# Optimization experiments

Hardware: AMD Instinct MI355X
Metric: run time of the kernel (lower is better)

## Reference

```python
import jax, jax.numpy as jnp
import numpy as np

H, L, N1, N2, N3 = 256, 141, 9, 34, 98
B, S = 64, 512

def setup_inputs() -> dict:
    key = jax.random.key(0)
    cnt = [0]
    def nrm(shape, s=0.05):
        cnt[0] += 1
        return jax.random.normal(jax.random.fold_in(key, cnt[0]), shape, jnp.float32) * s
    d = {}
    d['inputs'] = jax.random.randint(jax.random.fold_in(key, 1000), (B, S), 0, 30522)
    d['text_hidden'] = nrm((B, S, 768), 1.0)
    d['label_encoding'] = nrm((L, H), 1.0)
    d['w12'] = (jax.random.uniform(jax.random.fold_in(key, 1001), (N1, N2)) < 0.3).astype(jnp.float32)
    d['w23'] = (jax.random.uniform(jax.random.fold_in(key, 1002), (N2, N3)) < 0.3).astype(jnp.float32)
    d['fre12'] = jax.random.uniform(jax.random.fold_in(key, 1003), (N1, N2), jnp.float32)
    d['fre23'] = jax.random.uniform(jax.random.fold_in(key, 1004), (N2, N3), jnp.float32)
    for name in ['wi1', 'wf1', 'wo1', 'wu1', 'wi2', 'wf2', 'wo2', 'wu2']:
        d[name + '_W'] = nrm((H, H)); d[name + '_b'] = nrm((H,))
    for name in ['ui1', 'uf1', 'uo1', 'uu1', 'ui2', 'uf2', 'uo2', 'uu2']:
        d[name + '_W'] = nrm((H, H))
    d['mix_W'] = nrm((3 * H, H)); d['mix_b'] = nrm((H,))
    d['tt_W'] = nrm((768, H)); d['tt_b'] = nrm((H,))
    d['A'] = nrm((L, L)); d['Wp'] = nrm((H, H))
    d['out_W'] = nrm((L * H, L)); d['out_b'] = nrm((L,))
    return d

def reference(inputs, text_hidden, label_encoding, w12, w23, fre12, fre23,
              wi1_W, wi1_b, wf1_W, wf1_b, wo1_W, wo1_b, wu1_W, wu1_b,
              wi2_W, wi2_b, wf2_W, wf2_b, wo2_W, wo2_b, wu2_W, wu2_b,
              ui1_W, uf1_W, uo1_W, uu1_W, ui2_W, uf2_W, uo2_W, uu2_W,
              mix_W, mix_b, tt_W, tt_b, A, Wp, out_W, out_b):
    sig, tanh = jax.nn.sigmoid, jnp.tanh
    v1 = label_encoding[:N1]          # [N1,H]
    v2 = label_encoding[N1:N1 + N2]   # [N2,H]
    v3 = label_encoding[N1 + N2:]     # [N3,H]
    w21, w32 = w12.T, w23.T
    # --- top-down tree-LSTM (suffix 1) ---
    i11 = sig(v1 @ wi1_W + wi1_b); o11 = sig(v1 @ wo1_W + wo1_b); u11 = tanh(v1 @ wu1_W + wu1_b)
    c11 = i11 * u11; h11 = o11 * tanh(c11)
    h21t = w21 @ h11
    i21 = sig(v2 @ wi1_W + wi1_b + h21t @ ui1_W)
    f21 = sig(v2 @ wf1_W + wf1_b + h21t @ uf1_W)
    o21 = sig(v2 @ wo1_W + wo1_b + h21t @ uo1_W)
    u21 = tanh(v2 @ wu1_W + wu1_b + h21t @ uu1_W)
    c21 = i21 * u21 + f21 * (w21 @ c11); h21 = o21 * tanh(c21)
    h31t = w32 @ h21
    i31 = sig(v3 @ wi1_W + wi1_b + h31t @ ui1_W)
    f31 = sig(v3 @ wf1_W + wf1_b + h31t @ uf1_W)
    o31 = sig(v3 @ wo1_W + wo1_b + h31t @ uo1_W)
    u31 = tanh(v3 @ wu1_W + wu1_b + h31t @ uu1_W)
    c31 = i31 * u31 + f31 * (w32 @ c21); h31 = o31 * tanh(c31)
    # --- bottom-up tree-LSTM (suffix 2) ---
    i32 = sig(v3 @ wi2_W + wi2_b); o32 = sig(v3 @ wo2_W + wo2_b); u32 = tanh(v3 @ wu2_W + wu2_b)
    c32 = i32 * u32; h32 = o32 * tanh(c32)
    h22t = fre23 @ h32
    i22 = sig(v2 @ wi2_W + wi2_b + h22t @ ui2_W)
    f22 = sig((w32 @ v2) @ wf2_W + wf2_b + h32 @ uf2_W)   # [N3,H]
    o22 = sig(v2 @ wo2_W + wo2_b + h22t @ uo2_W)
    u22 = tanh(v2 @ wu2_W + wu2_b + h22t @ uu2_W)
    c22 = i22 * u22 + w23 @ (f22 * c32); h22 = o22 * tanh(c22)
    h12t = fre12 @ h22
    i12 = sig(v1 @ wi2_W + wi2_b + h12t @ ui2_W)
    f12 = sig((w21 @ v1) @ wf2_W + wf2_b + h22 @ uf2_W)   # [N2,H]
    o12 = sig(v1 @ wo2_W + wo2_b + h12t @ uo2_W)
    u12 = tanh(v1 @ wu2_W + wu2_b + h12t @ uu2_W)
    c12 = i12 * u12 + w12 @ (f12 * c22); h12 = o12 * tanh(c12)
    h1 = jnp.concatenate([h11, h12], axis=1)
    h2 = jnp.concatenate([h21, h22], axis=1)
    h3 = jnp.concatenate([h31, h32], axis=1)
    le = jnp.concatenate([h1, h2, h3], axis=0)            # [L,2H]
    temp = jax.nn.relu(A @ label_encoding @ Wp)           # [L,H]
    le = jnp.concatenate([le, temp], axis=1) @ mix_W + mix_b  # [L,H]
    # --- masked cross-attention pooling over text ---
    text = tanh(text_hidden @ tt_W + tt_b)                # [B,S,H]
    att = jnp.einsum('lh,bsh->bls', le, text)             # [B,L,S]
    pad = jnp.where((inputs == 0) | (inputs == 101) | (inputs == 102), -jnp.inf, 0.0).astype(text.dtype)
    att = jax.nn.softmax(att + pad[:, None, :], axis=2)
    features = jnp.einsum('bls,bsh->blh', att, text).reshape(inputs.shape[0], -1)  # [B,L*H]
    return sig(features @ out_W + out_b)                  # [B,L]
```

## Files before the change

kernel.cpp:

```cpp
#include <hip/hip_runtime.h>
#include <math.h>

static constexpr int H = 256, L = 141, N1 = 9, N2 = 34, N3 = 98;
static constexpr int B = 64, S = 512;

typedef __attribute__((ext_vector_type(8))) _Float16 f16x8;
typedef __attribute__((ext_vector_type(4))) float f32x4;

__device__ inline unsigned short f2h(float x) {
    _Float16 h = (_Float16)x;
    return __builtin_bit_cast(unsigned short, h);
}
__device__ inline float sigf(float x) { return 1.f / (1.f + __expf(-x)); }

__device__ inline void gload_lds16(const void* g, void* l) {
    __builtin_amdgcn_global_load_lds(
        (const __attribute__((address_space(1))) void*)g,
        (__attribute__((address_space(3))) void*)l, 16, 0, 0);
}

__global__ __launch_bounds__(256) void conv_ttW(
    const float* __restrict__ W, unsigned short* __restrict__ Bt)
{
    __shared__ unsigned short Tl[32][257];
    const int t = blockIdx.x, tid = threadIdx.x;
    #pragma unroll
    for (int p = 0; p < 32; p++) {
        int lin = p * 256 + tid;
        int r = lin >> 8, c = lin & 255;
        Tl[r][c] = f2h(W[(long)(t * 32 + r) * 256 + c]);
    }
    __syncthreads();
    unsigned short v[32];
    #pragma unroll
    for (int kin = 0; kin < 32; kin++) v[kin] = Tl[kin][tid];
    uint4* dst = (uint4*)(Bt + ((long)t * 256 + tid) * 32);
    #pragma unroll
    for (int q = 0; q < 4; q++) dst[q] = ((const uint4*)v)[q];
}

__global__ __launch_bounds__(512, 4) void text_gemm3(
    const float* __restrict__ Af,
    const unsigned short* __restrict__ Bt,
    const float* __restrict__ bias,
    unsigned short* __restrict__ outH,
    unsigned short* __restrict__ outHT)
{
    __shared__ unsigned short smem[28672];
    unsigned short* As = smem;
    unsigned short* Bs = smem + 4096;
    unsigned short* T  = smem;

    const int tid  = threadIdx.x;
    const int wave = tid >> 6, lane = tid & 63;
    const int quad = lane >> 4, l16 = lane & 15;
    const int m0 = blockIdx.x * 64;
    const int wm = (wave >> 2) * 32;
    const int wn = (wave & 3) * 64;

    const int arow = tid >> 3;
    const int ac16 = tid & 7;
    const float* aSrc = Af + (long)(m0 + arow) * 768 + ac16 * 4;
    const int ac8d = ac16 ^ ((arow & 3) << 1);
    const int aWoff = arow * 32 + ac8d * 4;

    const int bsc = (lane & 3) ^ ((lane >> 3) & 3);
    const long bSrcOff0 = (long)(wave * 32 + (lane >> 2)) * 32 + bsc * 8;
    const long bSrcOff1 = bSrcOff0 + 16 * 32;
    const int bDst0 = (wave * 32) * 32, bDst1 = (wave * 32 + 16) * 32;

    int aro[2], bro[4];
    #pragma unroll
    for (int i = 0; i < 2; i++) {
        int r = wm + i * 16 + l16;
        aro[i] = r * 32 + ((quad * 2) ^ ((r & 3) << 1)) * 4;
    }
    #pragma unroll
    for (int j = 0; j < 4; j++) {
        int n = wn + j * 16 + l16;
        bro[j] = n * 32 + ((quad ^ ((n >> 1) & 3)) << 3);
    }

    f32x4 acc[2][4] = {};
    float4 ar0, ar1;

    auto issueB = [&](int kt, int pb) {
        const unsigned short* src = Bt + (long)kt * 8192;
        unsigned short* d = Bs + pb * 8192;
        gload_lds16(src + bSrcOff0, d + bDst0);
        gload_lds16(src + bSrcOff1, d + bDst1);
    };
    auto writeA = [&](const float4& v, int pa) {
        unsigned int p0 = f2h(v.x) | ((unsigned int)f2h(v.y) << 16);
        unsigned int p1 = f2h(v.z) | ((unsigned int)f2h(v.w) << 16);
        *(uint2*)&As[pa * 2048 + aWoff] = make_uint2(p0, p1);
    };

    ar0 = *(const float4*)(aSrc + 0 * 32);
    issueB(0, 0);
    ar1 = *(const float4*)(aSrc + 1 * 32);
    issueB(1, 1);
    asm volatile("s_waitcnt vmcnt(5)" ::: "memory");
    writeA(ar0, 0);
    asm volatile("s_waitcnt vmcnt(3)" ::: "memory");
    asm volatile("s_waitcnt lgkmcnt(0)" ::: "memory");
    asm volatile("s_barrier" ::: "memory");

    auto body = [&](int t, float4& arIn, float4& arOut, int pa, int pr) {
        int kt2 = (t + 2 <= 23) ? t + 2 : 23;
        arOut = *(const float4*)(aSrc + kt2 * 32);
        f16x8 a[2], b[4];
        const unsigned short* ab = As + pa * 2048;
        const unsigned short* bb = Bs + pr * 8192;
        #pragma unroll
        for (int i = 0; i < 2; i++) a[i] = *(const f16x8*)&ab[aro[i]];
        #pragma unroll
        for (int j = 0; j < 4; j++) b[j] = *(const f16x8*)&bb[bro[j]];
        #pragma unroll
        for (int i = 0; i < 2; i++)
            #pragma unroll
            for (int j = 0; j < 4; j++)
                acc[i][j] = __builtin_amdgcn_mfma_f32_16x16x32_f16(
                    a[i], b[j], acc[i][j], 0, 0, 0);
        asm volatile("s_waitcnt vmcnt(3)" ::: "memory");
        writeA(arIn, pa ^ 1);
        int pw = pr + 2; if (pw >= 3) pw -= 3;
        issueB(kt2, pw);
        asm volatile("s_waitcnt vmcnt(3)" ::: "memory");
        asm volatile("s_waitcnt lgkmcnt(0)" ::: "memory");
        asm volatile("s_barrier" ::: "memory");
    };

    int pr = 0;
    #pragma unroll 1
    for (int t = 0; t < 24; t += 2) {
        body(t,     ar1, ar0, t & 1 ? 1 : 0, pr);
        int pr1 = pr + 1; if (pr1 >= 3) pr1 -= 3;
        body(t + 1, ar0, ar1, 1, pr1);
        pr = pr1 + 1; if (pr >= 3) pr -= 3;
    }
    asm volatile("s_waitcnt vmcnt(0)" ::: "memory");
    __syncthreads();

    float bv[4];
    #pragma unroll
    for (int j = 0; j < 4; j++) bv[j] = bias[wn + j * 16 + l16];

    #pragma unroll
    for (int i = 0; i < 2; i++) {
        #pragma unroll
        for (int j = 0; j < 4; j++) {
            const int mlb = wm + i * 16 + quad * 4;
            const int n   = wn + j * 16 + l16;
            unsigned short hv[4];
            #pragma unroll
            for (int r = 0; r < 4; r++) {
                float v = tanhf(acc[i][j][r] + bv[j]);
                hv[r] = f2h(v);
                outH[(long)(m0 + mlb + r) * 256 + n] = hv[r];
            }
            uint2 p;
            p.x = hv[0] | ((unsigned int)hv[1] << 16);
            p.y = hv[2] | ((unsigned int)hv[3] << 16);
            *(uint2*)&T[n * 72 + mlb] = p;
        }
    }
    __syncthreads();
    {
        const int bb2 = m0 >> 9, s0 = m0 & 511;
        const int n = tid >> 1, half = tid & 1;
        const uint4* src = (const uint4*)&T[n * 72 + half * 32];
        uint4* dst = (uint4*)&outHT[((long)bb2 * 256 + n) * 512 + s0 + half * 32];
        dst[0] = src[0]; dst[1] = src[1];
        dst[2] = src[2]; dst[3] = src[3];
    }
}

__global__ __launch_bounds__(512, 4) void att_logits(
    const unsigned short* __restrict__ le_h,
    const unsigned short* __restrict__ text_h,
    const int* __restrict__ tokens,
    float* __restrict__ att)
{
    __shared__ unsigned short A_s[64 * 256];
    __shared__ unsigned short Bs[3][256 * 32];
    const int tid  = threadIdx.x;
    const int wave = tid >> 6, lane = tid & 63;
    const int quad = lane >> 4, l16 = lane & 15;
    const int s0 = blockIdx.x * 256;
    const int m0 = blockIdx.y * 64;
    const int b  = blockIdx.z;
    const int wm = (wave >> 2) * 32;
    const int wn = (wave & 3) * 64;

    const int bsc = (lane & 3) ^ ((lane >> 3) & 3);
    const long bOff0 = (long)(b * 512 + s0 + wave * 32 + (lane >> 2)) * 256 + bsc * 8;
    const long bOff1 = bOff0 + 16 * 256;
    const int bDst0 = (wave * 32) * 32, bDst1 = bDst0 + 16 * 32;
    auto issueB = [&](int kt, int pb) {
        gload_lds16(text_h + bOff0 + kt * 32, &Bs[pb][bDst0]);
        gload_lds16(text_h + bOff1 + kt * 32, &Bs[pb][bDst1]);
    };

    int abase[2], axm[2], bro[4];
    #pragma unroll
    for (int i = 0; i < 2; i++) {
        int r = wm + i * 16 + l16;
        abase[i] = r * 256; axm[i] = r & 7;
    }
    #pragma unroll
    for (int j = 0; j < 4; j++) {
        int n = wn + j * 16 + l16;
        bro[j] = n * 32 + ((quad ^ ((n >> 1) & 3)) << 3);
    }

    #pragma unroll
    for (int p = 0; p < 4; p++) {
        int row = p * 16 + (tid >> 5);
        int c   = tid & 31;
        int grow = m0 + row; if (grow > L - 1) grow = L - 1;
        gload_lds16(le_h + (long)grow * 256 + ((c ^ (row & 7)) << 3),
                    A_s + p * 4096 + wave * 512);
    }
    issueB(0, 0);
    issueB(1, 1);
    asm volatile("s_waitcnt vmcnt(2)" ::: "memory");
    asm volatile("s_barrier" ::: "memory");

    f32x4 acc[2][4] = {};
    #pragma unroll 1
    for (int t = 0; t < 8; t++) {
        const int pr = t % 3;
        f16x8 a[2], b[4];
        #pragma unroll
        for (int i = 0; i < 2; i++)
            a[i] = *(const f16x8*)&A_s[abase[i] + (((t * 4 + quad) ^ axm[i]) << 3)];
        const unsigned short* bb = &Bs[pr][0];
        #pragma unroll
        for (int j = 0; j < 4; j++) b[j] = *(const f16x8*)&bb[bro[j]];
        #pragma unroll
        for (int i = 0; i < 2; i++)
            #pragma unroll
            for (int j = 0; j < 4; j++)
                acc[i][j] = __builtin_amdgcn_mfma_f32_16x16x32_f16(
                    a[i], b[j], acc[i][j], 0, 0, 0);
        if (t < 7) {
            int kt2 = (t + 2 <= 7) ? t + 2 : 7;
            int pw = (t + 2) % 3;
            issueB(kt2, pw);
            asm volatile("s_waitcnt vmcnt(2)" ::: "memory");
            asm volatile("s_barrier" ::: "memory");
        }
    }
    asm volatile("s_waitcnt vmcnt(0)" ::: "memory");

    float mvv[4];
    #pragma unroll
    for (int j = 0; j < 4; j++) {
        int gs = s0 + wn + j * 16 + l16;
        int tok = tokens[(long)b * 512 + gs];
        mvv[j] = (tok == 0 || tok == 101 || tok == 102) ? 1e30f : 0.f;
    }
    #pragma unroll
    for (int i = 0; i < 2; i++)
        #pragma unroll
        for (int j = 0; j < 4; j++)
            #pragma unroll
            for (int r = 0; r < 4; r++) {
                int gm = m0 + wm + i * 16 + quad * 4 + r;
                if (gm < L) {
                    int gs = s0 + wn + j * 16 + l16;
                    att[(long)b * (L * S) + (long)gm * 512 + gs] =
                        acc[i][j][r] - mvv[j];
                }
            }
}

template<int EPI, bool CONVA, int IM>
__global__ __launch_bounds__(256) void gemm_mfma(
    const void* __restrict__ Aptr, int lda, long strA,
    const unsigned short* __restrict__ Bp, int ldb, long strB,
    float* __restrict__ C, int ldc, long strC,
    int M, int N, int K,
    const float* __restrict__ bias,
    const int* __restrict__ tokens,
    unsigned short* __restrict__ outH,
    unsigned short* __restrict__ outHT,
    int kChunk)
{
    __shared__ unsigned short A_s[32 * IM * 32];
    __shared__ unsigned short B_s[128 * 32];
    const int tid  = threadIdx.x;
    const int wave = tid >> 6, lane = tid & 63;
    const int quad = lane >> 4, l16 = lane & 15;
    const int bz = blockIdx.z;
    const int m0 = blockIdx.y * (32 * IM), n0 = blockIdx.x * 128;
    const int wm = (wave & 1) * (16 * IM), wn = (wave >> 1) * 64;

    long aBase, bBase;
    int kBeg, kEnd;
    if (EPI == 4) { aBase = 0; bBase = 0; kBeg = bz * kChunk; kEnd = kBeg + kChunk; }
    else { aBase = (long)bz * strA; bBase = (long)bz * strB; kBeg = 0; kEnd = K; }

    f32x4 acc[IM][4] = {};

    for (int k0 = kBeg; k0 < kEnd; k0 += 32) {
        if (CONVA) {
            const float* Af = (const float*)Aptr + aBase;
            #pragma unroll
            for (int it = 0; it < IM; it++) {
                int idx = it * 256 + tid;
                int row = idx >> 3, col4 = idx & 7;
                int gm = m0 + row; if (gm > M - 1) gm = M - 1;
                float4 v = *(const float4*)(Af + (long)gm * lda + k0 + col4 * 4);
                unsigned int p0 = f2h(v.x) | ((unsigned int)f2h(v.y) << 16);
                unsigned int p1 = f2h(v.z) | ((unsigned int)f2h(v.w) << 16);
                *(uint2*)&A_s[row * 32 + col4 * 4] = make_uint2(p0, p1);
            }
        } else {
            const unsigned short* Ab = (const unsigned short*)Aptr + aBase;
            #pragma unroll
            for (int t = 0; t < IM / 2; t++) {
                int rowb = wave * (8 * IM) + t * 16;
                int gm = m0 + rowb + (lane >> 2); if (gm > M - 1) gm = M - 1;
                gload_lds16(Ab + (long)gm * lda + k0 + (lane & 3) * 8,
                            &A_s[rowb * 32]);
            }
        }
        #pragma unroll
        for (int t = 0; t < 2; t++) {
            int rowb = wave * 32 + t * 16;
            int gn = n0 + rowb + (lane >> 2); if (gn > N - 1) gn = N - 1;
            gload_lds16(Bp + bBase + (long)gn * ldb + k0 + (lane & 3) * 8,
                        &B_s[rowb * 32]);
        }
        __syncthreads();
        f16x8 a[IM], b[4];
        #pragma unroll
        for (int i = 0; i < IM; i++)
            a[i] = *(const f16x8*)&A_s[(wm + i * 16 + l16) * 32 + quad * 8];
        #pragma unroll
        for (int j = 0; j < 4; j++)
            b[j] = *(const f16x8*)&B_s[(wn + j * 16 + l16) * 32 + quad * 8];
        #pragma unroll
        for (int i = 0; i < IM; i++)
            #pragma unroll
            for (int j = 0; j < 4; j++)
                acc[i][j] = __builtin_amdgcn_mfma_f32_16x16x32_f16(
                    a[i], b[j], acc[i][j], 0, 0, 0);
        __syncthreads();
    }

    #pragma unroll
    for (int i = 0; i < IM; i++) {
        #pragma unroll
        for (int j = 0; j < 4; j++) {
            #pragma unroll
            for (int r = 0; r < 4; r++) {
                int ml = wm + i * 16 + quad * 4 + r;
                int nl = wn + j * 16 + l16;
                int gm = m0 + ml, gn = n0 + nl;
                if (gm >= M || gn >= N) continue;
                float v = acc[i][j][r];
                if (EPI == 2) {
                    int tok = tokens[(long)bz * 512 + gn];
                    if (tok == 0 || tok == 101 || tok == 102) v -= 1e30f;
                    C[(long)bz * strC + (long)gm * ldc + gn] = v;
                } else if (EPI == 3) {
                    outH[(long)bz * strC + (long)gm * ldc + gn] = f2h(v);
                } else {
                    C[(long)bz * strC + (long)gm * ldc + gn] = v;
                }
            }
        }
    }
}

__global__ __launch_bounds__(256) void transp_t64(
    const float* __restrict__ src, unsigned short* __restrict__ dst,
    int R, int C)
{
    __shared__ unsigned short T[64 * 65];
    const int tid = threadIdx.x;
    const int r0 = blockIdx.x * 64, c0 = blockIdx.y * 64;
    #pragma unroll
    for (int p = 0; p < 16; p++) {
        int lin = p * 256 + tid;
        int r = lin >> 6, c = lin & 63;
        int gc = c0 + c;
        float v = (gc < C) ? src[(long)(r0 + r) * C + gc] : 0.f;
        T[c * 65 + r] = f2h(v);
    }
    __syncthreads();
    #pragma unroll
    for (int p = 0; p < 16; p++) {
        int lin = p * 256 + tid;
        int c = lin >> 6, r = lin & 63;
        if (c0 + c < C)
            dst[(long)(c0 + c) * R + r0 + r] = T[c * 65 + r];
    }
}

__global__ __launch_bounds__(256) void gate_pre(
    const float* __restrict__ le,
    const float* W0, const float* W1, const float* W2, const float* W3,
    const float* W4, const float* W5, const float* W6,
    const float* b0, const float* b1, const float* b2, const float* b3,
    const float* b4, const float* b5, const float* b6,
    float* __restrict__ G)
{
    __shared__ float ls[256];
    __shared__ float red[256];
    const int j = blockIdx.x >> 2, x = blockIdx.x & 3, m = blockIdx.y;
    const int tid = threadIdx.x, nl = tid & 63, ks = tid >> 6, n = x * 64 + nl;
    ls[tid] = le[(long)m * 256 + tid];
    __syncthreads();
    const float *W, *bb;
    switch (j) {
        case 0: W = W0; bb = b0; break;  case 1: W = W1; bb = b1; break;
        case 2: W = W2; bb = b2; break;  case 3: W = W3; bb = b3; break;
        case 4: W = W4; bb = b4; break;  case 5: W = W5; bb = b5; break;
        default: W = W6; bb = b6;
    }
    float a0 = 0, a1 = 0, a2 = 0, a3 = 0;
    for (int k = ks; k + 12 < 256; k += 16) {
        long o = (long)k * 256 + n;
        a0 += ls[k] * W[o];        a1 += ls[k + 4] * W[o + 1024];
        a2 += ls[k + 8] * W[o + 2048]; a3 += ls[k + 12] * W[o + 3072];
    }
    red[tid] = a0 + a1 + a2 + a3;
    __syncthreads();
    if (ks == 0)
        G[((long)j * 141 + m) * 256 + n] =
            red[nl] + red[64 + nl] + red[128 + nl] + red[192 + nl] + bb[n];
}

__global__ __launch_bounds__(256) void pre2(
    const float* __restrict__ A, const float* __restrict__ le,
    const float* __restrict__ w23, const float* __restrict__ w12,
    const float* __restrict__ Wp, const float* __restrict__ wf2_W,
    float* __restrict__ tmpP, float* __restrict__ wv2f, float* __restrict__ wv1f)
{
    __shared__ float cs[141];
    __shared__ float t[256];
    __shared__ float red[256];
    const int x = blockIdx.x, y = blockIdx.y;
    const int tid = threadIdx.x, nl = tid & 63, ks = tid >> 6, n = x * 64 + nl;
    int job, m, K1;
    if (y < 141)      { job = 0; m = y;       K1 = 141; }
    else if (y < 239) { job = 1; m = y - 141; K1 = 34; }
    else              { job = 2; m = y - 239; K1 = 9; }
    if (tid < K1)
        cs[tid] = (job == 0) ? A[(long)m * 141 + tid]
                : (job == 1) ? w23[(long)tid * 98 + m]
                             : w12[(long)tid * 34 + m];
    __syncthreads();
    const float* s1 = (job == 1) ? le + 9 * 256 : le;
    float acc = 0;
    #pragma unroll 4
    for (int k = 0; k < K1; k++) acc += cs[k] * s1[(long)k * 256 + tid];
    t[tid] = acc;
    __syncthreads();
    const float* W = (job == 0) ? Wp : wf2_W;
    float a0 = 0, a1 = 0, a2 = 0, a3 = 0;
    for (int k = ks; k + 12 < 256; k += 16) {
        long o = (long)k * 256 + n;
        a0 += t[k] * W[o];        a1 += t[k + 4] * W[o + 1024];
        a2 += t[k + 8] * W[o + 2048]; a3 += t[k + 12] * W[o + 3072];
    }
    red[tid] = a0 + a1 + a2 + a3;
    __syncthreads();
    if (ks == 0) {
        float tot = red[nl] + red[64 + nl] + red[128 + nl] + red[192 + nl];
        if (job == 0)      tmpP[(long)m * 256 + n] = fmaxf(tot, 0.f);
        else if (job == 1) wv2f[(long)m * 256 + n] = tot;
        else               wv1f[(long)m * 256 + n] = tot;
    }
}

__global__ __launch_bounds__(256) void ew1(
    const float* __restrict__ G, float* __restrict__ h11, float* __restrict__ c11,
    float* __restrict__ h32, float* __restrict__ c32)
{
    int y = blockIdx.x, n = threadIdx.x;
    if (y < 9) {
        int m = y;
        float iv = sigf(G[(0L * 141 + m) * 256 + n]);
        float ov = sigf(G[(2L * 141 + m) * 256 + n]);
        float uv = tanhf(G[(3L * 141 + m) * 256 + n]);
        float cv = iv * uv;
        c11[m * 256 + n] = cv; h11[m * 256 + n] = ov * tanhf(cv);
    } else {
        int r = y - 9, grow = 43 + r;
        float iv = sigf(G[(4L * 141 + grow) * 256 + n]);
        float ov = sigf(G[(5L * 141 + grow) * 256 + n]);
        float uv = tanhf(G[(6L * 141 + grow) * 256 + n]);
        float cv = iv * uv;
        c32[r * 256 + n] = cv; h32[r * 256 + n] = ov * tanhf(cv);
    }
}

__global__ __launch_bounds__(256) void chain_mm(int phase,
    const float* __restrict__ w12, const float* __restrict__ w23,
    const float* __restrict__ fre23, const float* __restrict__ fre12,
    const float* __restrict__ h11, const float* __restrict__ c11,
    const float* __restrict__ h32,
    const float* __restrict__ h21, const float* __restrict__ c21,
    const float* __restrict__ h22,
    const float* __restrict__ wv2f, const float* __restrict__ wv1f,
    const float* __restrict__ wf2_b, const float* __restrict__ uf2_W,
    const float* __restrict__ c32, const float* __restrict__ c22,
    float* __restrict__ h21t, float* __restrict__ c21p,
    float* __restrict__ h22t, float* __restrict__ fcb,
    float* __restrict__ h31t, float* __restrict__ c31p,
    float* __restrict__ h12t, float* __restrict__ fc2b)
{
    __shared__ float cs[256];
    __shared__ float red[256];
    const int x = blockIdx.x, y = blockIdx.y;
    const int tid = threadIdx.x, nl = tid & 63, ks = tid >> 6, n = x * 64 + nl;
    int job, m;
    if (phase == 0) {
        if (y < 34)       { job = 0; m = y; }
        else if (y < 68)  { job = 1; m = y - 34; }
        else if (y < 102) { job = 2; m = y - 68; }
        else              { job = 3; m = y - 102; }
    } else {
        if (y < 98)       { job = 0; m = y; }
        else if (y < 196) { job = 1; m = y - 98; }
        else if (y < 205) { job = 2; m = y - 196; }
        else              { job = 3; m = y - 205; }
    }
    if (job < 3) {
        int K; const float* src; float* dst;
        if (phase == 0) {
            K = (job == 2) ? 98 : 9;
            src = (job == 0) ? h11 : (job == 1) ? c11 : h32;
            dst = (job == 0) ? h21t : (job == 1) ? c21p : h22t;
            if (tid < K)
                cs[tid] = (job == 2) ? fre23[(long)m * 98 + tid]
                                     : w12[(long)tid * 34 + m];
        } else {
            K = 34;
            src = (job == 0) ? h21 : (job == 1) ? c21 : h22;
            dst = (job == 0) ? h31t : (job == 1) ? c31p : h12t;
            if (tid < K)
                cs[tid] = (job == 2) ? fre12[(long)m * 34 + tid]
                                     : w23[(long)tid * 98 + m];
        }
        __syncthreads();
        float a0 = 0;
        for (int k = ks; k < K; k += 4) a0 += cs[k] * src[(long)k * 256 + n];
        red[tid] = a0;
        __syncthreads();
        if (ks == 0)
            dst[(long)m * 256 + n] = red[nl] + red[64 + nl] + red[128 + nl] + red[192 + nl];
    } else {
        const float* row = (phase == 0) ? h32 + m * 256 : h22 + m * 256;
        const float* pre = (phase == 0) ? wv2f : wv1f;
        const float* cm  = (phase == 0) ? c32 : c22;
        float* dst       = (phase == 0) ? fcb : fc2b;
        cs[tid] = row[tid];
        __syncthreads();
        float a0 = 0, a1 = 0, a2 = 0, a3 = 0;
        for (int k = ks; k + 12 < 256; k += 16) {
            long o = (long)k * 256 + n;
            a0 += cs[k] * uf2_W[o];        a1 += cs[k + 4] * uf2_W[o + 1024];
            a2 += cs[k + 8] * uf2_W[o + 2048]; a3 += cs[k + 12] * uf2_W[o + 3072];
        }
        red[tid] = a0 + a1 + a2 + a3;
        __syncthreads();
        if (ks == 0) {
            float tot = red[nl] + red[64 + nl] + red[128 + nl] + red[192 + nl]
                      + pre[(long)m * 256 + n] + wf2_b[n];
            dst[(long)m * 256 + n] = sigf(tot) * cm[(long)m * 256 + n];
        }
    }
}

__global__ __launch_bounds__(256) void lstm_fused(int phase,
    const float* __restrict__ G,
    const float* __restrict__ h21t, const float* __restrict__ c21p,
    const float* __restrict__ h22t, const float* __restrict__ fcb,
    const float* __restrict__ h31t, const float* __restrict__ c31p,
    const float* __restrict__ h12t, const float* __restrict__ fc2b,
    const float* __restrict__ w23, const float* __restrict__ w12,
    const float* __restrict__ ui1, const float* __restrict__ uf1,
    const float* __restrict__ uo1, const float* __restrict__ uu1,
    const float* __restrict__ ui2, const float* __restrict__ uo2,
    const float* __restrict__ uu2,
    float* __restrict__ h21, float* __restrict__ c21,
    float* __restrict__ h22, float* __restrict__ c22,
    float* __restrict__ h31, float* __restrict__ h12)
{
    __shared__ float hs[256];
    __shared__ float cs[128];
    __shared__ float red[1024];
    const int x = blockIdx.x, y = blockIdx.y;
    const int tid = threadIdx.x, nl = tid & 63, ks = tid >> 6, n = x * 64 + nl;
    bool modef; int m, grow, Kx = 0;
    const float *hrow, *U0, *U1, *U2, *U3 = nullptr, *Sx = nullptr, *cmod = nullptr;
    float *ho, *co = nullptr;
    if (phase == 0) {
        if (y < 34) { modef = true;  m = y;      grow = 9 + m;  hrow = h21t;
                      U0 = ui1; U1 = uf1; U2 = uo1; U3 = uu1; cmod = c21p; ho = h21; co = c21; }
        else        { modef = false; m = y - 34; grow = 9 + m;  hrow = h22t;
                      U0 = ui2; U1 = uo2; U2 = uu2; Sx = fcb; Kx = 98; ho = h22; co = c22;
                      if (tid < 98) cs[tid] = w23[(long)m * 98 + tid]; }
    } else {
        if (y < 98) { modef = true;  m = y;      grow = 43 + m; hrow = h31t;
                      U0 = ui1; U1 = uf1; U2 = uo1; U3 = uu1; cmod = c31p; ho = h31; co = nullptr; }
        else        { modef = false; m = y - 98; grow = m;      hrow = h12t;
                      U0 = ui2; U1 = uo2; U2 = uu2; Sx = fc2b; Kx = 34; ho = h12; co = nullptr;
                      if (tid < 34) cs[tid] = w12[(long)m * 34 + tid]; }
    }
    hs[tid] = hrow[(long)m * 256 + tid];
    __syncthreads();
    float a0 = 0, a1 = 0, a2 = 0, a3 = 0;
    if (modef) {
        for (int k = ks; k < 256; k += 4) {
            float xv = hs[k]; long o = (long)k * 256 + n;
            a0 += xv * U0[o]; a1 += xv * U1[o]; a2 += xv * U2[o]; a3 += xv * U3[o];
        }
    } else {
        for (int k = ks; k < 256; k += 4) {
            float xv = hs[k]; long o = (long)k * 256 + n;
            a0 += xv * U0[o]; a1 += xv * U1[o]; a2 += xv * U2[o];
        }
        for (int k = ks; k < Kx; k += 4) a3 += cs[k] * Sx[(long)k * 256 + n];
    }
    red[tid] = a0; red[256 + tid] = a1; red[512 + tid] = a2; red[768 + tid] = a3;
    __syncthreads();
    if (ks == 0) {
        float t0 = 0, t1 = 0, t2 = 0, t3 = 0;
        #pragma unroll
        for (int s2 = 0; s2 < 4; s2++) {
            t0 += red[s2 * 64 + nl];       t1 += red[256 + s2 * 64 + nl];
            t2 += red[512 + s2 * 64 + nl]; t3 += red[768 + s2 * 64 + nl];
        }
        if (modef) {
            float ti = t0 + G[(0L * 141 + grow) * 256 + n];
            float tf = t1 + G[(1L * 141 + grow) * 256 + n];
            float to = t2 + G[(2L * 141 + grow) * 256 + n];
            float tu = t3 + G[(3L * 141 + grow) * 256 + n];
            float cv = sigf(ti) * tanhf(tu) + sigf(tf) * cmod[(long)m * 256 + n];
            ho[(long)m * 256 + n] = sigf(to) * tanhf(cv);
            if (co) co[(long)m * 256 + n] = cv;
        } else {
            float ti = t0 + G[(4L * 141 + grow) * 256 + n];
            float to = t1 + G[(5L * 141 + grow) * 256 + n];
            float tu = t2 + G[(6L * 141 + grow) * 256 + n];
            float cv = sigf(ti) * tanhf(tu) + t3;
            ho[(long)m * 256 + n] = sigf(to) * tanhf(cv);
            if (co) co[(long)m * 256 + n] = cv;
        }
    }
}

__global__ __launch_bounds__(256) void mix_mm(
    const float* __restrict__ h11, const float* __restrict__ h12,
    const float* __restrict__ h21, const float* __restrict__ h22,
    const float* __restrict__ h31, const float* __restrict__ h32,
    const float* __restrict__ tmpP, const float* __restrict__ mix_W,
    const float* __restrict__ mix_b, unsigned short* __restrict__ le_h)
{
    __shared__ float ls[768];
    __shared__ float red[256];
    const int x = blockIdx.x, l = blockIdx.y;
    const int tid = threadIdx.x, nl = tid & 63, ks = tid >> 6, n = x * 64 + nl;
    const float *pa, *pb; int r;
    if (l < 9)       { pa = h11; pb = h12; r = l; }
    else if (l < 43) { pa = h21; pb = h22; r = l - 9; }
    else             { pa = h31; pb = h32; r = l - 43; }
    for (int j = tid; j < 768; j += 256) {
        float v;
        if (j < 256)      v = pa[r * 256 + j];
        else if (j < 512) v = pb[r * 256 + (j - 256)];
        else              v = tmpP[l * 256 + (j - 512)];
        ls[j] = v;
    }
    __syncthreads();
    float a0 = 0, a1 = 0, a2 = 0, a3 = 0;
    for (int k = ks; k + 12 < 768; k += 16) {
        long o = (long)k * 256 + n;
        a0 += ls[k] * mix_W[o];        a1 += ls[k + 4] * mix_W[o + 1024];
        a2 += ls[k + 8] * mix_W[o + 2048]; a3 += ls[k + 12] * mix_W[o + 3072];
    }
    red[tid] = a0 + a1 + a2 + a3;
    __syncthreads();
    if (ks == 0) {
        float tot = red[nl] + red[64 + nl] + red[128 + nl] + red[192 + nl] + mix_b[n];
        le_h[(long)l * 256 + n] = f2h(tot);
    }
}

__global__ __launch_bounds__(256) void softmax512(
    const float* __restrict__ att, unsigned short* __restrict__ atth)
{
    __shared__ float red[256];
    const float* row = att + (long)blockIdx.x * 512;
    unsigned short* orow = atth + (long)blockIdx.x * 512;
    int t = threadIdx.x;
    float a = row[t], b = row[t + 256];
    red[t] = fmaxf(a, b);
    __syncthreads();
    for (int s = 128; s > 0; s >>= 1) {
        if (t < s) red[t] = fmaxf(red[t], red[t + s]);
        __syncthreads();
    }
    float m = red[0];
    __syncthreads();
    float ea = __expf(a - m), eb = __expf(b - m);
    red[t] = ea + eb;
    __syncthreads();
    for (int s = 128; s > 0; s >>= 1) {
        if (t < s) red[t] += red[t + s];
        __syncthreads();
    }
    float inv = 1.f / red[0];
    orow[t] = f2h(ea * inv);
    orow[t + 256] = f2h(eb * inv);
}

__global__ __launch_bounds__(256) void out_final(
    const float* __restrict__ acc, const float* __restrict__ ob,
    float* __restrict__ out, int total, int nz)
{
    int i = blockIdx.x * 256 + threadIdx.x;
    if (i >= total) return;
    float v = ob[i % L];
    #pragma unroll 4
    for (int z = 0; z < nz; z++) v += acc[(long)z * total + i];
    out[i] = sigf(v);
}

extern "C" void kernel_launch(void* const* d_in, const int* in_sizes, int n_in,
                              void* d_out, int out_size, void* d_ws, size_t ws_size,
                              hipStream_t stream)
{
    (void)in_sizes; (void)n_in; (void)out_size; (void)ws_size;
    const int*   inputs      = (const int*)d_in[0];
    const float* text_hidden = (const float*)d_in[1];
    const float* label_enc   = (const float*)d_in[2];
    const float* w12   = (const float*)d_in[3];
    const float* w23   = (const float*)d_in[4];
    const float* fre12 = (const float*)d_in[5];
    const float* fre23 = (const float*)d_in[6];
    const float* wi1_W = (const float*)d_in[7],  *wi1_b = (const float*)d_in[8];
    const float* wf1_W = (const float*)d_in[9],  *wf1_b = (const float*)d_in[10];
    const float* wo1_W = (const float*)d_in[11], *wo1_b = (const float*)d_in[12];
    const float* wu1_W = (const float*)d_in[13], *wu1_b = (const float*)d_in[14];
    const float* wi2_W = (const float*)d_in[15], *wi2_b = (const float*)d_in[16];
    const float* wf2_W = (const float*)d_in[17], *wf2_b = (const float*)d_in[18];
    const float* wo2_W = (const float*)d_in[19], *wo2_b = (const float*)d_in[20];
    const float* wu2_W = (const float*)d_in[21], *wu2_b = (const float*)d_in[22];
    const float* ui1_W = (const float*)d_in[23], *uf1_W = (const float*)d_in[24];
    const float* uo1_W = (const float*)d_in[25], *uu1_W = (const float*)d_in[26];
    const float* ui2_W = (const float*)d_in[27], *uf2_W = (const float*)d_in[28];
    const float* uo2_W = (const float*)d_in[29], *uu2_W = (const float*)d_in[30];
    const float* mix_W = (const float*)d_in[31], *mix_b = (const float*)d_in[32];
    const float* tt_W  = (const float*)d_in[33], *tt_b  = (const float*)d_in[34];
    const float* Amat  = (const float*)d_in[35], *Wp    = (const float*)d_in[36];
    const float* out_W = (const float*)d_in[37], *out_b = (const float*)d_in[38];
    float* out = (float*)d_out;

    float* ws = (float*)d_ws;
    float* att     = ws; ws += (long)B * L * S;
    unsigned short* text_h  = (unsigned short*)ws; ws += (long)B * S * H / 2;
    unsigned short* text_hT = (unsigned short*)ws; ws += (long)B * S * H / 2;
    unsigned short* att_h   = (unsigned short*)ws; ws += (long)B * L * S / 2;
    unsigned short* tt_Wt   = (unsigned short*)ws; ws += 768 * H / 2;
    unsigned short* le_h    = (unsigned short*)ws; ws += L * H / 2 + 4;
    unsigned short* out_Wh  = (unsigned short*)ws; ws += (long)L * 36096 / 2;
    unsigned short* feat_h  = (unsigned short*)ws; ws += (long)B * L * H / 2;
    float* outacc = ws; ws += (long)B * L * 141;
    float* G    = ws; ws += 7 * 141 * 256;
    float* tmpP = ws; ws += L * H;
    float* wv2f = ws; ws += N3 * H;
    float* wv1f = ws; ws += N2 * H;
    float* h11  = ws; ws += N1 * H;  float* c11  = ws; ws += N1 * H;
    float* h21  = ws; ws += N2 * H;  float* c21  = ws; ws += N2 * H;
    float* h21t = ws; ws += N2 * H;  float* c21p = ws; ws += N2 * H;
    float* h31  = ws; ws += N3 * H;  float* h31t = ws; ws += N3 * H;
    float* c31p = ws; ws += N3 * H;
    float* h32  = ws; ws += N3 * H;  float* c32  = ws; ws += N3 * H;
    float* h22  = ws; ws += N2 * H;  float* c22  = ws; ws += N2 * H;
    float* h22t = ws; ws += N2 * H;  float* fcb  = ws; ws += N3 * H;
    float* h12  = ws; ws += N1 * H;  float* h12t = ws; ws += N1 * H;
    float* fc2b = ws; ws += N2 * H;

    conv_ttW<<<24, 256, 0, stream>>>(tt_W, tt_Wt);
    text_gemm3<<<512, 512, 0, stream>>>(
        text_hidden, tt_Wt, tt_b, text_h, text_hT);
    gate_pre<<<dim3(28, 141), 256, 0, stream>>>(label_enc,
        wi1_W, wf1_W, wo1_W, wu1_W, wi2_W, wo2_W, wu2_W,
        wi1_b, wf1_b, wo1_b, wu1_b, wi2_b, wo2_b, wu2_b, G);
    pre2<<<dim3(4, 273), 256, 0, stream>>>(Amat, label_enc, w23, w12, Wp, wf2_W,
        tmpP, wv2f, wv1f);
    transp_t64<<<dim3(36096 / 64, 3), 256, 0, stream>>>(out_W, out_Wh, 36096, 141);
    ew1<<<107, 256, 0, stream>>>(G, h11, c11, h32, c32);
    chain_mm<<<dim3(4, 200), 256, 0, stream>>>(0, w12, w23, fre23, fre12,
        h11, c11, h32, h21, c21, h22, wv2f, wv1f, wf2_b, uf2_W, c32, c22,
        h21t, c21p, h22t, fcb, h31t, c31p, h12t, fc2b);
    lstm_fused<<<dim3(4, 68), 256, 0, stream>>>(0, G,
        h21t, c21p, h22t, fcb, h31t, c31p, h12t, fc2b, w23, w12,
        ui1_W, uf1_W, uo1_W, uu1_W, ui2_W, uo2_W, uu2_W,
        h21, c21, h22, c22, h31, h12);
    chain_mm<<<dim3(4, 239), 256, 0, stream>>>(1, w12, w23, fre23, fre12,
        h11, c11, h32, h21, c21, h22, wv2f, wv1f, wf2_b, uf2_W, c32, c22,
        h21t, c21p, h22t, fcb, h31t, c31p, h12t, fc2b);
    lstm_fused<<<dim3(4, 107), 256, 0, stream>>>(1, G,
        h21t, c21p, h22t, fcb, h31t, c31p, h12t, fc2b, w23, w12,
        ui1_W, uf1_W, uo1_W, uu1_W, ui2_W, uo2_W, uu2_W,
        h21, c21, h22, c22, h31, h12);
    mix_mm<<<dim3(4, 141), 256, 0, stream>>>(h11, h12, h21, h22, h31, h32,
        tmpP, mix_W, mix_b, le_h);
    att_logits<<<dim3(2, 3, 64), 512, 0, stream>>>(
        le_h, text_h, inputs, att);
    softmax512<<<B * L, 256, 0, stream>>>(att, att_h);
    gemm_mfma<3, false, 2><<<dim3(H / 128, (L + 63) / 64, B), 256, 0, stream>>>(
        att_h, S, (long)L * S, text_hT, S, (long)H * S, nullptr, H, (long)L * H,
        L, H, S, nullptr, nullptr, feat_h, nullptr, 0);
    gemm_mfma<4, false, 2><<<dim3(2, 1, 141), 256, 0, stream>>>(
        feat_h, L * H, 0, out_Wh, L * H, 0, outacc, L, (long)B * L,
        B, L, L * H, nullptr, nullptr, nullptr, nullptr, 256);
    out_final<<<(B * L + 255) / 256, 256, 0, stream>>>(outacc, out_b, out, B * L, 141);
}
```

Measured before the change: 453.3 us.

## Add dedicated attention-times-text kernel with full-H tiles and async LDS pipeline

Replaces the generic MFMA GEMM for the attention-weighted pooling (att @ text) with a specialized kernel whose 64x256 output tile covers all of H per block. Loads go directly to LDS through global_load_lds with XOR swizzles, double-buffered for A and triple-buffered for B, so loads overlap the MFMA work. This is meant to cut redundant reloads of the attention rows across H tiles and to hide memory latency. It uses fewer, larger blocks (192), which may lower occupancy or leave CUs idle.

```diff
diff --git a/kernel.cpp b/kernel.cpp
--- a/kernel.cpp
+++ b/kernel.cpp
@@ -272,6 +272,106 @@
                     int gs = s0 + wn + j * 16 + l16;
                     att[(long)b * (L * S) + (long)gm * 512 + gs] =
                         acc[i][j][r] - mvv[j];
+                }
+            }
+}
+
+__global__ __launch_bounds__(512, 4) void att_pv(
+    const unsigned short* __restrict__ att_h,
+    const unsigned short* __restrict__ text_hT,
+    unsigned short* __restrict__ feat_h)
+{
+    __shared__ unsigned short As[2 * 64 * 64];
+    __shared__ unsigned short Bs[3][256 * 32];
+    const int tid  = threadIdx.x;
+    const int wave = tid >> 6, lane = tid & 63;
+    const int quad = lane >> 4, l16 = lane & 15;
+    const int m0 = blockIdx.x * 64;
+    const int b  = blockIdx.y;
+    const int wm = (wave >> 2) * 32;
+    const int wn = (wave & 3) * 64;
+
+    int arow = m0 + wave * 8 + (lane >> 3); if (arow > L - 1) arow = L - 1;
+    const int asc = (lane & 7) ^ (lane >> 3);
+    const unsigned short* aSrc = att_h + ((long)b * L + arow) * 512 + asc * 8;
+    const int aDst = wave * 512;
+    auto issueA = [&](int ka, int pa) {
+        gload_lds16(aSrc + ka * 64, &As[pa * 4096 + aDst]);
+    };
+
+    const int bsc = (lane & 3) ^ ((lane >> 3) & 3);
+    const long bOff0 = ((long)b * 256 + wave * 32 + (lane >> 2)) * 512 + bsc * 8;
+    const long bOff1 = bOff0 + 16 * 512;
+    const int bDst0 = (wave * 32) * 32, bDst1 = bDst0 + 16 * 32;
+    auto issueB = [&](int kt, int pb) {
+        gload_lds16(text_hT + bOff0 + kt * 32, &Bs[pb][bDst0]);
+        gload_lds16(text_hT + bOff1 + kt * 32, &Bs[pb][bDst1]);
+    };
+
+    int aro[2], axm[2], bro[4];
+    #pragma unroll
+    for (int i = 0; i < 2; i++) {
+        int r = wm + i * 16 + l16;
+        aro[i] = r * 64; axm[i] = r & 7;
+    }
+    #pragma unroll
+    for (int j = 0; j < 4; j++) {
+        int n = wn + j * 16 + l16;
+        bro[j] = n * 32 + ((quad ^ ((n >> 1) & 3)) << 3);
+    }
+
+    issueA(0, 0);
+    issueB(0, 0);
+    issueB(1, 1);
+    asm volatile("s_waitcnt vmcnt(2)" ::: "memory");
+    asm volatile("s_barrier" ::: "memory");
+
+    f32x4 acc[2][4] = {};
+    #pragma unroll 1
+    for (int t = 0; t < 16; t++) {
+        const int pa = (t >> 1) & 1, pr = t % 3, sub = t & 1;
+        f16x8 a[2], bfr[4];
+        const unsigned short* ab = &As[pa * 4096];
+        #pragma unroll
+        for (int i = 0; i < 2; i++)
+            a[i] = *(const f16x8*)&ab[aro[i] + (((sub * 4 + quad) ^ axm[i]) << 3)];
+        const unsigned short* bb = &Bs[pr][0];
+        #pragma unroll
+        for (int j = 0; j < 4; j++) bfr[j] = *(const f16x8*)&bb[bro[j]];
+        #pragma unroll
+        for (int i = 0; i < 2; i++)
+            #pragma unroll
+            for (int j = 0; j < 4; j++)
+                acc[i][j] = __builtin_amdgcn_mfma_f32_16x16x32_f16(
+                    a[i], bfr[j], acc[i][j], 0, 0, 0);
+        if (t < 15) {
+            if (sub == 0) {
+                int ka = (t >> 1) + 1; if (ka > 7) ka = 7;
+                issueA(ka, pa ^ 1);
+            }
+            int kb = t + 2; if (kb > 15) kb = 15;
+            issueB(kb, (t + 2) % 3);
+            if (sub == 0) {
+                asm volatile("s_waitcnt vmcnt(3)" ::: "memory");
+            } else {
+                asm volatile("s_waitcnt vmcnt(2)" ::: "memory");
+            }
+            asm volatile("s_barrier" ::: "memory");
+        }
+    }
+    asm volatile("s_waitcnt vmcnt(0)" ::: "memory");
+
+    #pragma unroll
+    for (int i = 0; i < 2; i++)
+        #pragma unroll
+        for (int j = 0; j < 4; j++)
+            #pragma unroll
+            for (int r = 0; r < 4; r++) {
+                int gm = m0 + wm + i * 16 + quad * 4 + r;
+                if (gm < L) {
+                    int h = wn + j * 16 + l16;
+                    feat_h[(long)b * (L * H) + (long)gm * 256 + h] =
+                        f2h(acc[i][j][r]);
                 }
             }
 }
@@ -818,9 +918,7 @@
     att_logits<<<dim3(2, 3, 64), 512, 0, stream>>>(
         le_h, text_h, inputs, att);
     softmax512<<<B * L, 256, 0, stream>>>(att, att_h);
-    gemm_mfma<3, false, 2><<<dim3(H / 128, (L + 63) / 64, B), 256, 0, stream>>>(
-        att_h, S, (long)L * S, text_hT, S, (long)H * S, nullptr, H, (long)L * H,
-        L, H, S, nullptr, nullptr, feat_h, nullptr, 0);
+    att_pv<<<dim3(3, 64), 512, 0, stream>>>(att_h, text_hT, feat_h);
     gemm_mfma<4, false, 2><<<dim3(2, 1, 141), 256, 0, stream>>>(
         feat_h, L * H, 0, out_Wh, L * H, 0, outacc, L, (long)B * L,
         B, L, L * H, nullptr, nullptr, nullptr, nullptr, 256);
```

Result: no change. 454.0 us (+0.1%).
